# Optimization experiments

Hardware: AMD Instinct MI355X
Metric: run time of the kernel (lower is better)

Reference implementation:

```python
import jax, jax.numpy as jnp
import numpy as np

B, Hh, Ww, C = 16, 56, 56, 384
HEADS, WS, SHIFT = 12, 7, 3
N = WS * WS            # 49 tokens per window
NW = (Hh // WS) * (Ww // WS)  # 64 windows
HID = int(C * 4.0)
SCALE = (C // HEADS) ** -0.5
EPS = 1e-5


def _relative_position_index():
    coords = np.stack(np.meshgrid(np.arange(WS), np.arange(WS), indexing='ij')).reshape(2, -1)
    rel = (coords[:, :, None] - coords[:, None, :]).transpose(1, 2, 0)  # (N,N,2)
    rel[..., 0] += WS - 1
    rel[..., 1] += WS - 1
    rel[..., 0] *= 2 * WS - 1
    return jnp.asarray(rel.sum(-1))  # (N,N) int

RPI = _relative_position_index()


def _swin_mask():
    img = np.zeros((Hh, Ww), np.float32)
    slices = (slice(0, -WS), slice(-WS, -SHIFT), slice(-SHIFT, None))
    cnt = 0
    for hs in slices:
        for ws in slices:
            img[hs, ws] = cnt
            cnt += 1
    m = img.reshape(Hh // WS, WS, Ww // WS, WS).transpose(0, 2, 1, 3).reshape(-1, N)  # (nW,N)
    am = m[:, None, :] - m[:, :, None]
    return jnp.asarray(np.where(am != 0, -100.0, 0.0).astype(np.float32))  # (nW,N,N)


def setup_inputs() -> dict:
    key = jax.random.key(0)
    ks = jax.random.split(key, 12)
    p = lambda k, shp, s=0.02: (jax.random.normal(k, shp, jnp.float32) * s)
    return {
        'x': jax.random.normal(ks[0], (B, Hh * Ww, C), jnp.float32),
        'mask_matrix': _swin_mask(),
        'norm1_g': jnp.ones((C,), jnp.float32),
        'norm1_b': jnp.zeros((C,), jnp.float32),
        'qkv_w': p(ks[1], (3 * C, C)),
        'qkv_b': jnp.zeros((3 * C,), jnp.float32),
        'rpb_table': p(ks[2], ((2 * WS - 1) * (2 * WS - 1), HEADS)),
        'proj_w': p(ks[3], (C, C)),
        'proj_b': jnp.zeros((C,), jnp.float32),
        'norm2_g': jnp.ones((C,), jnp.float32),
        'norm2_b': jnp.zeros((C,), jnp.float32),
        'fc1_w': p(ks[4], (HID, C)),
        'fc1_b': jnp.zeros((HID,), jnp.float32),
        'fc2_w': p(ks[5], (C, HID)),
        'fc2_b': jnp.zeros((C,), jnp.float32),
    }


def _ln(x, g, b):
    m = jnp.mean(x, -1, keepdims=True)
    v = jnp.mean(jnp.square(x - m), -1, keepdims=True)
    return (x - m) * jax.lax.rsqrt(v + EPS) * g + b


def reference(x, mask_matrix, norm1_g, norm1_b, qkv_w, qkv_b, rpb_table,
              proj_w, proj_b, norm2_g, norm2_b, fc1_w, fc1_b, fc2_w, fc2_b):
    shortcut = x
    h = _ln(x, norm1_g, norm1_b).reshape(B, Hh, Ww, C)
    # cyclic shift (H,W divisible by window -> no pad)
    h = jnp.roll(h, (-SHIFT, -SHIFT), axis=(1, 2))
    # window partition -> (B*nW, N, C)
    win = h.reshape(B, Hh // WS, WS, Ww // WS, WS, C).transpose(0, 1, 3, 2, 4, 5).reshape(-1, N, C)
    B_ = win.shape[0]
    hd = C // HEADS
    qkv = (win @ qkv_w.T + qkv_b).reshape(B_, N, 3, HEADS, hd).transpose(2, 0, 3, 1, 4)
    q, k, v = qkv[0] * SCALE, qkv[1], qkv[2]  # (B_,H,N,hd)
    attn = jnp.einsum('bhnd,bhmd->bhnm', q, k)  # (B_,H,N,N)
    bias = rpb_table[RPI]  # (N,N,heads)
    attn = attn + bias.transpose(2, 0, 1)[None]
    attn = attn.reshape(B, NW, HEADS, N, N) + mask_matrix[None, :, None]
    attn = jax.nn.softmax(attn.reshape(B_, HEADS, N, N), axis=-1)
    out = jnp.einsum('bhnm,bhmd->bhnd', attn, v).transpose(0, 2, 1, 3).reshape(B_, N, C)
    out = out @ proj_w.T + proj_b
    # window reverse + reverse shift
    out = out.reshape(B, Hh // WS, Ww // WS, WS, WS, C).transpose(0, 1, 3, 2, 4, 5).reshape(B, Hh, Ww, C)
    out = jnp.roll(out, (SHIFT, SHIFT), axis=(1, 2)).reshape(B, Hh * Ww, C)
    x = shortcut + out
    h2 = _ln(x, norm2_g, norm2_b)
    h2 = jax.nn.gelu(h2 @ fc1_w.T + fc1_b, approximate=False)  # torch nn.GELU exact
    return x + (h2 @ fc2_w.T + fc2_b)
```

## Files before the change

### kernel.cpp

```cpp
#include <hip/hip_runtime.h>

typedef unsigned short u16;
typedef unsigned int u32;
typedef short s16x8 __attribute__((ext_vector_type(8)));
typedef unsigned short u16x4 __attribute__((ext_vector_type(4)));
typedef float f32x4 __attribute__((ext_vector_type(4)));
typedef float f32x2 __attribute__((ext_vector_type(2)));

#define ATTN_SCALE 0.17677669529663687f

__device__ __forceinline__ u16 f2bf(float f) {
  union { float f; u32 i; } c; c.f = f;
  u32 r = c.i + 0x7fffu + ((c.i >> 16) & 1u);
  return (u16)(r >> 16);
}
__device__ __forceinline__ float bf2f(u16 u) {
  union { u32 i; float f; } c; c.i = ((u32)u) << 16; return c.f;
}
__device__ __forceinline__ f32x4 mfma16(s16x8 a, s16x8 b, f32x4 c) {
  return __builtin_amdgcn_mfma_f32_16x16x32_bf16(a, b, c, 0, 0, 0);
}

typedef __attribute__((address_space(1))) u32 gas_u32;
typedef __attribute__((address_space(3))) u32 las_u32;
#define GLL16(gp, lp) __builtin_amdgcn_global_load_lds((gas_u32*)(gp), (las_u32*)(lp), 16, 0, 0)

__device__ __forceinline__ int win_to_orig(int m) {
  int b = m / 3136, rem = m - b * 3136;
  int w = rem / 49, n = rem - w * 49;
  int wh = w >> 3, ww = w & 7;
  int i = n / 7, j = n - i * 7;
  int r = wh * 7 + i + 3; if (r >= 56) r -= 56;
  int c = ww * 7 + j + 3; if (c >= 56) c -= 56;
  return b * 3136 + r * 56 + c;
}

__global__ __launch_bounds__(256) void cvt_all_kernel(
    const float* __restrict__ qkvw, const float* __restrict__ projw,
    const float* __restrict__ fc1w, const float* __restrict__ fc2w,
    u16* __restrict__ wq, u16* __restrict__ wp,
    u16* __restrict__ w1, u16* __restrict__ w2) {
  int i = blockIdx.x * 256 + threadIdx.x;
  if (i < 442368) wq[i] = f2bf(qkvw[i]);
  else if (i < 589824) wp[i - 442368] = f2bf(projw[i - 442368]);
  else if (i < 1179648) w1[i - 589824] = f2bf(fc1w[i - 589824]);
  else if (i < 1769472) w2[i - 1179648] = f2bf(fc2w[i - 1179648]);
}

__global__ __launch_bounds__(256) void mk_tbl_kernel(
    const float* __restrict__ rpb, const float* __restrict__ maskp,
    u16* __restrict__ tbl) {
  int idx = blockIdx.x * 256 + threadIdx.x;
  int wh = idx >> 12;
  int rem = idx & 4095;
  int irow = rem >> 6;
  int lr = (rem >> 2) & 15, ni = rem & 3;
  int j = ni * 16 + lr;
  int wi = wh / 12, h = wh - wi * 12;
  float val = -1e30f;
  if (irow < 49 && j < 49) {
    int yi = irow / 7, xi = irow - yi * 7;
    int yj = j / 7, xj = j - yj * 7;
    int rpi = (yi - yj + 6) * 13 + (xi - xj + 6);
    val = rpb[rpi * 12 + h] + maskp[((size_t)wi * 49 + irow) * 49 + j];
  }
  tbl[idx] = f2bf(val);
}

template <bool PERM, bool BFIN>
__global__ __launch_bounds__(256) void ln_kernel(
    const void* __restrict__ xin, const float* __restrict__ g,
    const float* __restrict__ bb, u16* __restrict__ xo) {
  int t = blockIdx.x * 4 + (threadIdx.x >> 6);
  int l = threadIdx.x & 63;
  int src = PERM ? win_to_orig(t) : t;
  float v0[3], v1[3];
  if (BFIN) {
    const u32* row = (const u32*)((const u16*)xin + (size_t)src * 384);
#pragma unroll
    for (int k = 0; k < 3; k++) {
      u32 pr = row[l + 64 * k];
      v0[k] = bf2f((u16)pr);
      v1[k] = bf2f((u16)(pr >> 16));
    }
  } else {
    const float* row = (const float*)xin + (size_t)src * 384;
#pragma unroll
    for (int k = 0; k < 3; k++) {
      f32x2 pr = *(const f32x2*)(row + 2 * (l + 64 * k));
      v0[k] = pr[0]; v1[k] = pr[1];
    }
  }
  float s = 0.f;
#pragma unroll
  for (int k = 0; k < 3; k++) s += v0[k] + v1[k];
#pragma unroll
  for (int d = 1; d < 64; d <<= 1) s += __shfl_xor(s, d);
  float mean = s * (1.f / 384.f);
  float q = 0.f;
#pragma unroll
  for (int k = 0; k < 3; k++) {
    float d0 = v0[k] - mean, d1 = v1[k] - mean;
    q += d0 * d0 + d1 * d1;
  }
#pragma unroll
  for (int d = 1; d < 64; d <<= 1) q += __shfl_xor(q, d);
  float rstd = rsqrtf(q * (1.f / 384.f) + 1e-5f);
  u32* orow = (u32*)(xo + (size_t)t * 384);
#pragma unroll
  for (int k = 0; k < 3; k++) {
    int p = l + 64 * k;
    f32x2 gg = *(const f32x2*)(g + 2 * p);
    f32x2 bv = *(const f32x2*)(bb + 2 * p);
    u32 o0 = f2bf((v0[k] - mean) * rstd * gg[0] + bv[0]);
    u32 o1 = f2bf((v1[k] - mean) * rstd * gg[1] + bv[1]);
    orow[p] = o0 | (o1 << 16);
  }
}

template <int EPI>
__device__ __forceinline__ void gemm_epi(
    float v, size_t m, int col, int N, int dst,
    u16* __restrict__ outb, float* __restrict__ outf,
    const float* __restrict__ auxf, const u16* __restrict__ auxb) {
  if (EPI == 0) {
    outb[m * (size_t)N + col] = f2bf(v);
  } else if (EPI == 1) {
    outb[(size_t)dst * 384 + col] = f2bf(v + auxf[(size_t)dst * 384 + col]);
  } else if (EPI == 2) {
    float u = v * (0.7978845608028654f + 0.0356774081f * v * v);
    float gl = v / (1.f + __expf(-2.f * u));
    outb[m * (size_t)N + col] = f2bf(gl);
  } else {
    outf[m * (size_t)N + col] = v + bf2f(auxb[m * (size_t)N + col]);
  }
}

template <int EPI>
__global__ __launch_bounds__(256) void gemm128_kernel(
    const u16* __restrict__ A, const u16* __restrict__ W,
    const float* __restrict__ bias, u16* __restrict__ outb,
    float* __restrict__ outf, const float* __restrict__ auxf,
    const u16* __restrict__ auxb, int K, int N, int NT, int NB) {
  __shared__ __align__(16) short As[8192];
  __shared__ __align__(16) short Bs[8192];
  const int tid = threadIdx.x, wv = tid >> 6, l = tid & 63;
  const int lr = l & 15, lg = l >> 4;
  int bm, bn;
  {
    const int STS = NT << 3;
    const int body = (NB >> 3) * STS;
    int d = blockIdx.x;
    if (d < body) {
      int st = d / STS, rem = d - st * STS;
      bn = rem >> 3;
      bm = st * 8 + (rem & 7);
    } else {
      int t = d - body;
      int tq = t / NT;
      bm = (NB & ~7) + tq;
      bn = t - tq * NT;
    }
  }
  const size_t m0 = (size_t)bm * 128, n0 = (size_t)bn * 128;
  const int prow = wv * 16 + (l >> 2);
  const int ccl = (((l & 3) ^ ((l >> 3) & 3)) << 3);
  const u16* ga0 = A + (m0 + prow) * K + ccl;
  const u16* ga1 = A + (m0 + 64 + prow) * K + ccl;
  const u16* gb0 = W + (n0 + prow) * K + ccl;
  const u16* gb1 = W + (n0 + 64 + prow) * K + ccl;
  const int stoff = wv * 512;
  const int wr = wv >> 1, wc = wv & 1;
  const int sw = (lr >> 1) & 3;
  const int aoff = (wr * 64 + lr) * 32 + ((lg ^ sw) << 3);
  const int boff = (wc * 64 + lr) * 32 + ((lg ^ sw) << 3);

#define STAGE(bufo, koff)                            \
  do {                                               \
    GLL16(ga0 + (koff), As + (bufo) + stoff);        \
    GLL16(ga1 + (koff), As + (bufo) + 2048 + stoff); \
    GLL16(gb0 + (koff), Bs + (bufo) + stoff);        \
    GLL16(gb1 + (koff), Bs + (bufo) + 2048 + stoff); \
  } while (0)
#define FRAG_READS(cur)                                              \
  do {                                                               \
    const short* as = As + (cur);                                    \
    const short* bs = Bs + (cur);                                    \
    _Pragma("unroll") for (int mi = 0; mi < 4; mi++)                 \
        af[mi] = *(const s16x8*)&as[aoff + mi * 512];                \
    _Pragma("unroll") for (int ni = 0; ni < 4; ni++)                 \
        bfr[ni] = *(const s16x8*)&bs[boff + ni * 512];               \
  } while (0)
#define MFMA_TILE()                                        \
  do {                                                     \
    _Pragma("unroll") for (int mi = 0; mi < 4; mi++)       \
        _Pragma("unroll") for (int ni = 0; ni < 4; ni++)   \
            acc[mi][ni] = mfma16(af[mi], bfr[ni], acc[mi][ni]); \
  } while (0)

  f32x4 acc[4][4] = {};
  s16x8 af[4], bfr[4];
  STAGE(0, 0);
  STAGE(4096, 32);
  int cur = 0;
  int k0 = 0;
  for (; k0 < K - 32; k0 += 32) {
    asm volatile("s_waitcnt vmcnt(4)" ::: "memory");
    __builtin_amdgcn_sched_barrier(0);
    __builtin_amdgcn_s_barrier();
    FRAG_READS(cur);
    asm volatile("s_waitcnt lgkmcnt(0)" ::: "memory");
    __builtin_amdgcn_sched_barrier(0);
    __builtin_amdgcn_s_barrier();
    if (k0 + 64 < K) STAGE(cur, k0 + 64);
    MFMA_TILE();
    cur ^= 4096;
  }
  asm volatile("s_waitcnt vmcnt(0)" ::: "memory");
  __builtin_amdgcn_sched_barrier(0);
  __builtin_amdgcn_s_barrier();
  FRAG_READS(cur);
  asm volatile("s_waitcnt lgkmcnt(0)" ::: "memory");
  __builtin_amdgcn_sched_barrier(0);
  MFMA_TILE();
#undef STAGE
#undef FRAG_READS
#undef MFMA_TILE

  const int colb = (int)n0 + wc * 64;
#pragma unroll
  for (int mi = 0; mi < 4; mi++) {
#pragma unroll
    for (int r = 0; r < 4; r++) {
      const size_t m = m0 + wr * 64 + mi * 16 + lg * 4 + r;
      int dst = 0;
      if (EPI == 1) dst = win_to_orig((int)m);
#pragma unroll
      for (int ni = 0; ni < 4; ni++) {
        const int col = colb + ni * 16 + lr;
        gemm_epi<EPI>(acc[mi][ni][r] + bias[col], m, col, N, dst,
                      outb, outf, auxf, auxb);
      }
    }
  }
}

template <int EPI>
__global__ __launch_bounds__(512) void gemm256_kernel(
    const u16* __restrict__ A, const u16* __restrict__ W,
    const float* __restrict__ bias, u16* __restrict__ outb,
    float* __restrict__ outf, const float* __restrict__ auxf,
    const u16* __restrict__ auxb, int K, int N, int NT, int NB) {
  __shared__ __align__(16) short As[16384];
  __shared__ __align__(16) short Bs[8192];
  const int tid = threadIdx.x, wv = tid >> 6, l = tid & 63;
  const int lr = l & 15, lg = l >> 4;
  int bm, bn;
  {
    const int STS = NT << 3;
    const int body = (NB >> 3) * STS;
    int d = blockIdx.x;
    if (d < body) {
      int st = d / STS, rem = d - st * STS;
      bn = rem >> 3;
      bm = st * 8 + (rem & 7);
    } else {
      int t = d - body;
      int tq = t / NT;
      bm = (NB & ~7) + tq;
      bn = t - tq * NT;
    }
  }
  const size_t m0 = (size_t)bm * 256, n0 = (size_t)bn * 128;
  const int prow = wv * 16 + (l >> 2);
  const int ccl = (((l & 3) ^ ((l >> 3) & 3)) << 3);
  const u16* ga0 = A + (m0 + prow) * K + ccl;
  const u16* ga1 = A + (m0 + 128 + prow) * K + ccl;
  const u16* gb0 = W + (n0 + prow) * K + ccl;
  const int stoff = wv * 512;
  const int wr = wv >> 2, wc = wv & 3;
  const int sw = (lr >> 1) & 3;
  const int aoff = (wr * 128 + lr) * 32 + ((lg ^ sw) << 3);
  const int boff = (wc * 32 + lr) * 32 + ((lg ^ sw) << 3);

#define STAGE(c, koff)                                     \
  do {                                                     \
    GLL16(ga0 + (koff), As + (c) * 8192 + stoff);          \
    GLL16(ga1 + (koff), As + (c) * 8192 + 4096 + stoff);   \
    GLL16(gb0 + (koff), Bs + (c) * 4096 + stoff);          \
  } while (0)
#define FRAG_READS(c)                                                \
  do {                                                               \
    const short* as = As + (c) * 8192;                               \
    const short* bs = Bs + (c) * 4096;                               \
    _Pragma("unroll") for (int mi = 0; mi < 8; mi++)                 \
        af[mi] = *(const s16x8*)&as[aoff + mi * 512];                \
    _Pragma("unroll") for (int ni = 0; ni < 2; ni++)                 \
        bfr[ni] = *(const s16x8*)&bs[boff + ni * 512];               \
  } while (0)
#define MFMA_TILE()                                        \
  do {                                                     \
    __builtin_amdgcn_s_setprio(1);                         \
    _Pragma("unroll") for (int mi = 0; mi < 8; mi++)       \
        _Pragma("unroll") for (int ni = 0; ni < 2; ni++)   \
            acc[mi][ni] = mfma16(af[mi], bfr[ni], acc[mi][ni]); \
    __builtin_amdgcn_s_setprio(0);                         \
  } while (0)

  f32x4 acc[8][2] = {};
  s16x8 af[8], bfr[2];
  STAGE(0, 0);
  STAGE(1, 32);
  int cur = 0;
  int k0 = 0;
  for (; k0 < K - 32; k0 += 32) {
    asm volatile("s_waitcnt vmcnt(3)" ::: "memory");
    __builtin_amdgcn_sched_barrier(0);
    __builtin_amdgcn_s_barrier();
    FRAG_READS(cur);
    asm volatile("s_waitcnt lgkmcnt(0)" ::: "memory");
    __builtin_amdgcn_sched_barrier(0);
    __builtin_amdgcn_s_barrier();
    if (k0 + 64 < K) STAGE(cur, k0 + 64);
    MFMA_TILE();
    cur ^= 1;
  }
  asm volatile("s_waitcnt vmcnt(0)" ::: "memory");
  __builtin_amdgcn_sched_barrier(0);
  __builtin_amdgcn_s_barrier();
  FRAG_READS(cur);
  asm volatile("s_waitcnt lgkmcnt(0)" ::: "memory");
  __builtin_amdgcn_sched_barrier(0);
  MFMA_TILE();
#undef STAGE
#undef FRAG_READS
#undef MFMA_TILE

  const int colb = (int)n0 + wc * 32;
#pragma unroll
  for (int mi = 0; mi < 8; mi++) {
#pragma unroll
    for (int r = 0; r < 4; r++) {
      const size_t m = m0 + wr * 128 + mi * 16 + lg * 4 + r;
      int dst = 0;
      if (EPI == 1) dst = win_to_orig((int)m);
#pragma unroll
      for (int ni = 0; ni < 2; ni++) {
        const int col = colb + ni * 16 + lr;
        gemm_epi<EPI>(acc[mi][ni][r] + bias[col], m, col, N, dst,
                      outb, outf, auxf, auxb);
      }
    }
  }
}

__global__ __launch_bounds__(256) void attn_kernel(
    const u16* __restrict__ qkv, const u16* __restrict__ tbl,
    u16* __restrict__ out) {
  __shared__ __align__(16) short Pl[4][16 * 76];
  const int tid = threadIdx.x, wv = tid >> 6, l = tid & 63;
  const int lr = l & 15, lg = l >> 4;

  const int task = blockIdx.x * 4 + wv;
  const int win = task / 12, h = task - win * 12;
  const int wi = win & 63;
  const short* base = (const short*)qkv + (size_t)win * 49 * 1152 + h * 32;
  const u16* tb = tbl + (size_t)(wi * 12 + h) * 4096 + lr * 4;

  s16x8 qf[4], kf[4];
  const s16x8 zz = {0, 0, 0, 0, 0, 0, 0, 0};
#pragma unroll
  for (int mi = 0; mi < 4; mi++) {
    int n = mi * 16 + lr;
    if (n < 49) {
      qf[mi] = *(const s16x8*)(base + (size_t)n * 1152 + lg * 8);
      kf[mi] = *(const s16x8*)(base + (size_t)n * 1152 + 384 + lg * 8);
    } else { qf[mi] = zz; kf[mi] = zz; }
  }
  s16x8 vb[2][2];
#pragma unroll
  for (int kk = 0; kk < 2; kk++)
#pragma unroll
    for (int nd = 0; nd < 2; nd++)
#pragma unroll
      for (int e = 0; e < 8; e++)
        vb[kk][nd][e] = base[(size_t)(kk * 32 + lg * 8 + e) * 1152 + 768 + nd * 16 + lr];
  u16x4 t4[4][4];
#pragma unroll
  for (int r = 0; r < 4; r++)
    t4[0][r] = *(const u16x4*)&tb[(lg * 4 + r) * 64];

  f32x4 acc[4][4] = {};
  __builtin_amdgcn_s_setprio(1);
#pragma unroll
  for (int mi = 0; mi < 4; mi++)
#pragma unroll
    for (int ni = 0; ni < 4; ni++)
      acc[mi][ni] = mfma16(qf[mi], kf[ni], acc[mi][ni]);
  __builtin_amdgcn_s_setprio(0);

  short* pl = Pl[wv];
#pragma unroll
  for (int mi = 0; mi < 4; mi++) {
    if (mi < 3) {
#pragma unroll
      for (int r = 0; r < 4; r++)
        t4[mi + 1][r] = *(const u16x4*)&tb[((mi + 1) * 16 + lg * 4 + r) * 64];
    }
    float rs[4];
#pragma unroll
    for (int r = 0; r < 4; r++) {
      float sv[4];
#pragma unroll
      for (int ni = 0; ni < 4; ni++)
        sv[ni] = acc[mi][ni][r] * ATTN_SCALE + bf2f(t4[mi][r][ni]);
      float mx = fmaxf(fmaxf(sv[0], sv[1]), fmaxf(sv[2], sv[3]));
#pragma unroll
      for (int d = 1; d < 16; d <<= 1) mx = fmaxf(mx, __shfl_xor(mx, d));
      float sm = 0.f;
#pragma unroll
      for (int ni = 0; ni < 4; ni++) { sv[ni] = __expf(sv[ni] - mx); sm += sv[ni]; }
#pragma unroll
      for (int d = 1; d < 16; d <<= 1) sm += __shfl_xor(sm, d);
      rs[r] = 1.f / sm;
#pragma unroll
      for (int ni = 0; ni < 4; ni++)
        pl[(lg * 4 + r) * 76 + ni * 16 + lr] = (short)f2bf(sv[ni]);
    }
    f32x4 o[2] = {{}, {}};
    __builtin_amdgcn_s_setprio(1);
#pragma unroll
    for (int kk = 0; kk < 2; kk++) {
      s16x8 pa = *(const s16x8*)&pl[lr * 76 + kk * 32 + lg * 8];
#pragma unroll
      for (int nd = 0; nd < 2; nd++)
        o[nd] = mfma16(pa, vb[kk][nd], o[nd]);
    }
    __builtin_amdgcn_s_setprio(0);
#pragma unroll
    for (int r = 0; r < 4; r++) {
      const int irow = mi * 16 + lg * 4 + r;
      if (irow < 49) {
#pragma unroll
        for (int nd = 0; nd < 2; nd++)
          out[((size_t)win * 49 + irow) * 384 + h * 32 + nd * 16 + lr] =
              f2bf(o[nd][r] * rs[r]);
      }
    }
  }
}

extern "C" void kernel_launch(void* const* d_in, const int* in_sizes, int n_in,
                              void* d_out, int out_size, void* d_ws, size_t ws_size,
                              hipStream_t stream) {
  (void)in_sizes; (void)n_in; (void)out_size; (void)ws_size;
  const float* x     = (const float*)d_in[0];
  const float* maskp = (const float*)d_in[1];
  const float* n1g   = (const float*)d_in[2];
  const float* n1b   = (const float*)d_in[3];
  const float* qkvw  = (const float*)d_in[4];
  const float* qkvb  = (const float*)d_in[5];
  const float* rpb   = (const float*)d_in[6];
  const float* projw = (const float*)d_in[7];
  const float* projb = (const float*)d_in[8];
  const float* n2g   = (const float*)d_in[9];
  const float* n2b   = (const float*)d_in[10];
  const float* fc1w  = (const float*)d_in[11];
  const float* fc1b  = (const float*)d_in[12];
  const float* fc2w  = (const float*)d_in[13];
  const float* fc2b  = (const float*)d_in[14];
  float* outp = (float*)d_out;

  char* ws = (char*)d_ws;
  u16*  regA  = (u16*)ws;
  u16*  regB  = (u16*)(ws + 154140672ull);
  u16*  tbl   = (u16*)(ws + 192675840ull);
  u16*  xresb = (u16*)(ws + 192675840ull);
  u16*  wq = (u16*)(ws + 231211008ull);
  u16*  wp = wq + 442368;
  u16*  w1 = wp + 147456;
  u16*  w2 = w1 + 589824;

  cvt_all_kernel<<<6912, 256, 0, stream>>>(qkvw, projw, fc1w, fc2w, wq, wp, w1, w2);
  mk_tbl_kernel<<<12288, 256, 0, stream>>>(rpb, maskp, tbl);
  ln_kernel<true, false><<<12544, 256, 0, stream>>>(x, n1g, n1b, regB);
  gemm256_kernel<0><<<196 * 9, 512, 0, stream>>>(regB, wq, qkvb, regA, nullptr,
                                                 nullptr, nullptr, 384, 1152, 9, 196);
  attn_kernel<<<3072, 256, 0, stream>>>(regA, tbl, regB);
  gemm128_kernel<1><<<392 * 3, 256, 0, stream>>>(regB, wp, projb, xresb, nullptr,
                                                 x, nullptr, 384, 384, 3, 392);
  ln_kernel<false, true><<<12544, 256, 0, stream>>>(xresb, n2g, n2b, regB);
  gemm256_kernel<2><<<196 * 12, 512, 0, stream>>>(regB, w1, fc1b, regA, nullptr,
                                                  nullptr, nullptr, 384, 1536, 12, 196);
  gemm128_kernel<3><<<392 * 3, 256, 0, stream>>>(regA, w2, fc2b, nullptr, outp,
                                                 nullptr, xresb, 1536, 384, 3, 392);
}
```

Before: 425.8 us.

## Replace 256x128 GEMM with triple-buffered 64-wide K tile, 2x4 wave layout

```diff
diff --git a/kernel.cpp b/kernel.cpp
--- a/kernel.cpp
+++ b/kernel.cpp
@@ -133,6 +133,135 @@
     outb[m * (size_t)N + col] = f2bf(gl);
   } else {
     outf[m * (size_t)N + col] = v + bf2f(auxb[m * (size_t)N + col]);
+  }
+}
+
+template <int EPI>
+__global__ __launch_bounds__(512) void gemm8p_kernel(
+    const u16* __restrict__ A, const u16* __restrict__ W,
+    const float* __restrict__ bias, u16* __restrict__ outb,
+    float* __restrict__ outf, const float* __restrict__ auxf,
+    const u16* __restrict__ auxb, int K, int N, int NT, int NB) {
+  __shared__ __align__(16) short As[3 * 16384];
+  __shared__ __align__(16) short Bs[3 * 8192];
+  const int tid = threadIdx.x, wv = tid >> 6, l = tid & 63;
+  const int lr = l & 15, lg = l >> 4;
+  int bm, bn;
+  {
+    const int STS = NT << 3;
+    const int body = (NB >> 3) * STS;
+    int d = blockIdx.x;
+    if (d < body) {
+      int st = d / STS, rem = d - st * STS;
+      bn = rem >> 3;
+      bm = st * 8 + (rem & 7);
+    } else {
+      int t = d - body;
+      int tq = t / NT;
+      bm = (NB & ~7) + tq;
+      bn = t - tq * NT;
+    }
+  }
+  const size_t m0 = (size_t)bm * 256, n0 = (size_t)bn * 128;
+  const int srow = wv * 8 + (l >> 3);
+  const int schk = ((l & 7) ^ (l >> 3)) << 3;
+  const u16* gaA = A + (m0 + srow) * K + schk;
+  const u16* gaB = W + (n0 + srow) * K + schk;
+  const int stoff = wv * 512;
+  const int wr = wv >> 1, wc = wv & 1;
+  const int rsw = (lr & 7) << 3;
+
+  const int nt = K >> 6;
+#pragma unroll
+  for (int tt = 0; tt < 2; ++tt) {
+#pragma unroll
+    for (int r = 0; r < 4; r++)
+      GLL16(gaA + (size_t)r * 64 * K + tt * 64, As + tt * 16384 + r * 4096 + stoff);
+#pragma unroll
+    for (int r = 0; r < 2; r++)
+      GLL16(gaB + (size_t)r * 64 * K + tt * 64, Bs + tt * 8192 + r * 4096 + stoff);
+  }
+
+  f32x4 acc[4][4] = {};
+  s16x8 af[2][2], bfr[4][2];
+  for (int t = 0; t < nt; ++t) {
+    const int bt = t % 3;
+    const int st = t + 2, sb = st % 3;
+    const short* as = As + bt * 16384;
+    const short* bs = Bs + bt * 8192;
+    if (t + 1 < nt) { asm volatile("s_waitcnt vmcnt(6)" ::: "memory"); }
+    else            { asm volatile("s_waitcnt vmcnt(0)" ::: "memory"); }
+    __builtin_amdgcn_sched_barrier(0);
+    __builtin_amdgcn_s_barrier();
+    if (st < nt) {
+      GLL16(gaA + st * 64, As + sb * 16384 + stoff);
+      GLL16(gaA + (size_t)64 * K + st * 64, As + sb * 16384 + 4096 + stoff);
+      GLL16(gaB + st * 64, Bs + sb * 8192 + stoff);
+    }
+#pragma unroll
+    for (int ni = 0; ni < 4; ni++)
+#pragma unroll
+      for (int kk = 0; kk < 2; kk++)
+        bfr[ni][kk] = *(const s16x8*)&bs[(wc * 64 + ni * 16 + lr) * 64 +
+                                         (((kk * 4 + lg) << 3) ^ rsw)];
+#pragma unroll
+    for (int mi = 0; mi < 2; mi++)
+#pragma unroll
+      for (int kk = 0; kk < 2; kk++)
+        af[mi][kk] = *(const s16x8*)&as[(wr * 64 + mi * 16 + lr) * 64 +
+                                        (((kk * 4 + lg) << 3) ^ rsw)];
+    asm volatile("s_waitcnt lgkmcnt(0)" ::: "memory");
+    __builtin_amdgcn_sched_barrier(0);
+    __builtin_amdgcn_s_setprio(1);
+#pragma unroll
+    for (int mi = 0; mi < 2; mi++)
+#pragma unroll
+      for (int ni = 0; ni < 4; ni++)
+#pragma unroll
+        for (int kk = 0; kk < 2; kk++)
+          acc[mi][ni] = mfma16(af[mi][kk], bfr[ni][kk], acc[mi][ni]);
+    __builtin_amdgcn_s_setprio(0);
+    __builtin_amdgcn_s_barrier();
+    if (st < nt) {
+      GLL16(gaA + (size_t)128 * K + st * 64, As + sb * 16384 + 8192 + stoff);
+      GLL16(gaA + (size_t)192 * K + st * 64, As + sb * 16384 + 12288 + stoff);
+      GLL16(gaB + (size_t)64 * K + st * 64, Bs + sb * 8192 + 4096 + stoff);
+    }
+#pragma unroll
+    for (int mi = 0; mi < 2; mi++)
+#pragma unroll
+      for (int kk = 0; kk < 2; kk++)
+        af[mi][kk] = *(const s16x8*)&as[(wr * 64 + (mi + 2) * 16 + lr) * 64 +
+                                        (((kk * 4 + lg) << 3) ^ rsw)];
+    asm volatile("s_waitcnt lgkmcnt(0)" ::: "memory");
+    __builtin_amdgcn_sched_barrier(0);
+    __builtin_amdgcn_s_setprio(1);
+#pragma unroll
+    for (int mi = 0; mi < 2; mi++)
+#pragma unroll
+      for (int ni = 0; ni < 4; ni++)
+#pragma unroll
+        for (int kk = 0; kk < 2; kk++)
+          acc[mi + 2][ni] = mfma16(af[mi][kk], bfr[ni][kk], acc[mi + 2][ni]);
+    __builtin_amdgcn_s_setprio(0);
+    __builtin_amdgcn_s_barrier();
+  }
+
+  const int colb = (int)n0 + wc * 64;
+#pragma unroll
+  for (int mi = 0; mi < 4; mi++) {
+#pragma unroll
+    for (int r = 0; r < 4; r++) {
+      const size_t m = m0 + wr * 64 + mi * 16 + lg * 4 + r;
+      int dst = 0;
+      if (EPI == 1) dst = win_to_orig((int)m);
+#pragma unroll
+      for (int ni = 0; ni < 4; ni++) {
+        const int col = colb + ni * 16 + lr;
+        gemm_epi<EPI>(acc[mi][ni][r] + bias[col], m, col, N, dst,
+                      outb, outf, auxf, auxb);
+      }
+    }
   }
 }
 
@@ -245,115 +374,6 @@
   }
 }
 
-template <int EPI>
-__global__ __launch_bounds__(512) void gemm256_kernel(
-    const u16* __restrict__ A, const u16* __restrict__ W,
-    const float* __restrict__ bias, u16* __restrict__ outb,
-    float* __restrict__ outf, const float* __restrict__ auxf,
-    const u16* __restrict__ auxb, int K, int N, int NT, int NB) {
-  __shared__ __align__(16) short As[16384];
-  __shared__ __align__(16) short Bs[8192];
-  const int tid = threadIdx.x, wv = tid >> 6, l = tid & 63;
-  const int lr = l & 15, lg = l >> 4;
-  int bm, bn;
-  {
-    const int STS = NT << 3;
-    const int body = (NB >> 3) * STS;
-    int d = blockIdx.x;
-    if (d < body) {
-      int st = d / STS, rem = d - st * STS;
-      bn = rem >> 3;
-      bm = st * 8 + (rem & 7);
-    } else {
-      int t = d - body;
-      int tq = t / NT;
-      bm = (NB & ~7) + tq;
-      bn = t - tq * NT;
-    }
-  }
-  const size_t m0 = (size_t)bm * 256, n0 = (size_t)bn * 128;
-  const int prow = wv * 16 + (l >> 2);
-  const int ccl = (((l & 3) ^ ((l >> 3) & 3)) << 3);
-  const u16* ga0 = A + (m0 + prow) * K + ccl;
-  const u16* ga1 = A + (m0 + 128 + prow) * K + ccl;
-  const u16* gb0 = W + (n0 + prow) * K + ccl;
-  const int stoff = wv * 512;
-  const int wr = wv >> 2, wc = wv & 3;
-  const int sw = (lr >> 1) & 3;
-  const int aoff = (wr * 128 + lr) * 32 + ((lg ^ sw) << 3);
-  const int boff = (wc * 32 + lr) * 32 + ((lg ^ sw) << 3);
-
-#define STAGE(c, koff)                                     \
-  do {                                                     \
-    GLL16(ga0 + (koff), As + (c) * 8192 + stoff);          \
-    GLL16(ga1 + (koff), As + (c) * 8192 + 4096 + stoff);   \
-    GLL16(gb0 + (koff), Bs + (c) * 4096 + stoff);          \
-  } while (0)
-#define FRAG_READS(c)                                                \
-  do {                                                               \
-    const short* as = As + (c) * 8192;                               \
-    const short* bs = Bs + (c) * 4096;                               \
-    _Pragma("unroll") for (int mi = 0; mi < 8; mi++)                 \
-        af[mi] = *(const s16x8*)&as[aoff + mi * 512];                \
-    _Pragma("unroll") for (int ni = 0; ni < 2; ni++)                 \
-        bfr[ni] = *(const s16x8*)&bs[boff + ni * 512];               \
-  } while (0)
-#define MFMA_TILE()                                        \
-  do {                                                     \
-    __builtin_amdgcn_s_setprio(1);                         \
-    _Pragma("unroll") for (int mi = 0; mi < 8; mi++)       \
-        _Pragma("unroll") for (int ni = 0; ni < 2; ni++)   \
-            acc[mi][ni] = mfma16(af[mi], bfr[ni], acc[mi][ni]); \
-    __builtin_amdgcn_s_setprio(0);                         \
-  } while (0)
-
-  f32x4 acc[8][2] = {};
-  s16x8 af[8], bfr[2];
-  STAGE(0, 0);
-  STAGE(1, 32);
-  int cur = 0;
-  int k0 = 0;
-  for (; k0 < K - 32; k0 += 32) {
-    asm volatile("s_waitcnt vmcnt(3)" ::: "memory");
-    __builtin_amdgcn_sched_barrier(0);
-    __builtin_amdgcn_s_barrier();
-    FRAG_READS(cur);
-    asm volatile("s_waitcnt lgkmcnt(0)" ::: "memory");
-    __builtin_amdgcn_sched_barrier(0);
-    __builtin_amdgcn_s_barrier();
-    if (k0 + 64 < K) STAGE(cur, k0 + 64);
-    MFMA_TILE();
-    cur ^= 1;
-  }
-  asm volatile("s_waitcnt vmcnt(0)" ::: "memory");
-  __builtin_amdgcn_sched_barrier(0);
-  __builtin_amdgcn_s_barrier();
-  FRAG_READS(cur);
-  asm volatile("s_waitcnt lgkmcnt(0)" ::: "memory");
-  __builtin_amdgcn_sched_barrier(0);
-  MFMA_TILE();
-#undef STAGE
-#undef FRAG_READS
-#undef MFMA_TILE
-
-  const int colb = (int)n0 + wc * 32;
-#pragma unroll
-  for (int mi = 0; mi < 8; mi++) {
-#pragma unroll
-    for (int r = 0; r < 4; r++) {
-      const size_t m = m0 + wr * 128 + mi * 16 + lg * 4 + r;
-      int dst = 0;
-      if (EPI == 1) dst = win_to_orig((int)m);
-#pragma unroll
-      for (int ni = 0; ni < 2; ni++) {
-        const int col = colb + ni * 16 + lr;
-        gemm_epi<EPI>(acc[mi][ni][r] + bias[col], m, col, N, dst,
-                      outb, outf, auxf, auxb);
-      }
-    }
-  }
-}
-
 __global__ __launch_bounds__(256) void attn_kernel(
     const u16* __restrict__ qkv, const u16* __restrict__ tbl,
     u16* __restrict__ out) {
@@ -484,14 +504,14 @@
   cvt_all_kernel<<<6912, 256, 0, stream>>>(qkvw, projw, fc1w, fc2w, wq, wp, w1, w2);
   mk_tbl_kernel<<<12288, 256, 0, stream>>>(rpb, maskp, tbl);
   ln_kernel<true, false><<<12544, 256, 0, stream>>>(x, n1g, n1b, regB);
-  gemm256_kernel<0><<<196 * 9, 512, 0, stream>>>(regB, wq, qkvb, regA, nullptr,
-                                                 nullptr, nullptr, 384, 1152, 9, 196);
+  gemm8p_kernel<0><<<196 * 9, 512, 0, stream>>>(regB, wq, qkvb, regA, nullptr,
+                                                nullptr, nullptr, 384, 1152, 9, 196);
   attn_kernel<<<3072, 256, 0, stream>>>(regA, tbl, regB);
   gemm128_kernel<1><<<392 * 3, 256, 0, stream>>>(regB, wp, projb, xresb, nullptr,
                                                  x, nullptr, 384, 384, 3, 392);
   ln_kernel<false, true><<<12544, 256, 0, stream>>>(xresb, n2g, n2b, regB);
-  gemm256_kernel<2><<<196 * 12, 512, 0, stream>>>(regB, w1, fc1b, regA, nullptr,
-                                                  nullptr, nullptr, 384, 1536, 12, 196);
+  gemm8p_kernel<2><<<196 * 12, 512, 0, stream>>>(regB, w1, fc1b, regA, nullptr,
+                                                 nullptr, nullptr, 384, 1536, 12, 196);
   gemm128_kernel<3><<<392 * 3, 256, 0, stream>>>(regA, w2, fc2b, nullptr, outp,
                                                  nullptr, xresb, 1536, 384, 3, 392);
 }
```

After: 483.9 us. 1.14x slower.
